# Kernel tuning notes

Measured on AMD Instinct MI355X. Metric: run time of the kernel, lower is better.

Reference implementation:

```python
import jax, jax.numpy as jnp
import numpy as np

D_MODEL = 1024
H = 16
D_K = D_MODEL // H
WINDOW = 256
NEG = -1.0e9


def setup_inputs() -> dict:
    key = jax.random.key(0)
    ks = jax.random.split(key, 12)
    B, S = 1, 4096
    scale = 1.0 / np.sqrt(D_MODEL)
    inp = {
        'q': jax.random.normal(ks[0], (B, S, D_MODEL), dtype=jnp.float32),
        'k': jax.random.normal(ks[1], (B, S, D_MODEL), dtype=jnp.float32),
        'v': jax.random.normal(ks[2], (B, S, D_MODEL), dtype=jnp.float32),
        'w_q': jax.random.normal(ks[3], (D_MODEL, D_MODEL), dtype=jnp.float32) * scale,
        'b_q': jnp.zeros((D_MODEL,), dtype=jnp.float32),
        'w_k': jax.random.normal(ks[4], (D_MODEL, D_MODEL), dtype=jnp.float32) * scale,
        'b_k': jnp.zeros((D_MODEL,), dtype=jnp.float32),
        'w_v': jax.random.normal(ks[5], (D_MODEL, D_MODEL), dtype=jnp.float32) * scale,
        'b_v': jnp.zeros((D_MODEL,), dtype=jnp.float32),
        'w_o': jax.random.normal(ks[6], (D_MODEL, D_MODEL), dtype=jnp.float32) * scale,
        'b_o': jnp.zeros((D_MODEL,), dtype=jnp.float32),
    }
    return inp


def _local_mask(seq_len: int, window_size: int) -> jnp.ndarray:
    left = (window_size - 1) // 2
    right = window_size - 1 - left
    row = jnp.arange(seq_len)[:, None]
    col = jnp.arange(seq_len)[None, :]
    return (col >= row - left) & (col <= row + right)  # [S, S] bool


def reference(q, k, v, w_q, b_q, w_k, b_k, w_v, b_v, w_o, b_o):
    B, Sq, _ = q.shape
    Sk = k.shape[1]
    # projections (torch Linear: x @ W.T + b) -> [B, h, S, d_k]
    query = (q @ w_q.T + b_q).reshape(B, Sq, H, D_K).transpose(0, 2, 1, 3)
    key = (k @ w_k.T + b_k).reshape(B, Sk, H, D_K).transpose(0, 2, 1, 3)
    value = (v @ w_v.T + b_v).reshape(B, Sk, H, D_K).transpose(0, 2, 1, 3)

    scores = jnp.einsum('bhqd,bhkd->bhqk', query, key) / jnp.sqrt(
        jnp.asarray(D_K, dtype=query.dtype))
    if Sq == Sk:
        mask = _local_mask(Sq, WINDOW)  # [S, S]
        scores = jnp.where(mask[None, None], scores, jnp.asarray(NEG, scores.dtype))
    attn = jax.nn.softmax(scores, axis=-1)
    x = jnp.einsum('bhqk,bhkd->bhqd', attn, value)
    x = x.transpose(0, 2, 1, 3).reshape(B, Sq, D_MODEL)
    return x @ w_o.T + b_o
```

## Files before the change

kernel.cpp:

```cpp
#include <hip/hip_runtime.h>

#define SEQ 4096
#define DM 1024
#define NH 16
#define DK 64

typedef _Float16 half8 __attribute__((ext_vector_type(8)));
typedef _Float16 half4v __attribute__((ext_vector_type(4)));
typedef float f32x4 __attribute__((ext_vector_type(4)));

#define MFMA16(a, b, c) __builtin_amdgcn_mfma_f32_16x16x32_f16((a), (b), (c), 0, 0, 0)
#define GLOAD_LDS(g, l)                                                                  \
    __builtin_amdgcn_global_load_lds((const __attribute__((address_space(1))) void*)(g), \
                                     (__attribute__((address_space(3))) void*)(l), 16, 0, 0)

__device__ __forceinline__ float dpp_max16(float x) {
    x = fmaxf(x, __int_as_float(__builtin_amdgcn_update_dpp(
                     0, __float_as_int(x), 0xB1, 0xF, 0xF, true)));
    x = fmaxf(x, __int_as_float(__builtin_amdgcn_update_dpp(
                     0, __float_as_int(x), 0x4E, 0xF, 0xF, true)));
    x = fmaxf(x, __int_as_float(__builtin_amdgcn_update_dpp(
                     0, __float_as_int(x), 0x124, 0xF, 0xF, true)));
    x = fmaxf(x, __int_as_float(__builtin_amdgcn_update_dpp(
                     0, __float_as_int(x), 0x128, 0xF, 0xF, true)));
    return x;
}

__global__ void cvt_all(const float* __restrict__ q, const float* __restrict__ k,
                        const float* __restrict__ v, const float* __restrict__ wq,
                        const float* __restrict__ wk, const float* __restrict__ wv,
                        const float* __restrict__ wo, _Float16* __restrict__ qh,
                        _Float16* __restrict__ kh, _Float16* __restrict__ vh,
                        _Float16* __restrict__ wqh, _Float16* __restrict__ wkh,
                        _Float16* __restrict__ wvh, _Float16* __restrict__ woh) {
    int z = blockIdx.y;
    const float* src;
    _Float16* dst;
    int n;
    switch (z) {
    case 0: src = q;  dst = qh;  n = SEQ * DM; break;
    case 1: src = k;  dst = kh;  n = SEQ * DM; break;
    case 2: src = v;  dst = vh;  n = SEQ * DM; break;
    case 3: src = wq; dst = wqh; n = DM * DM;  break;
    case 4: src = wk; dst = wkh; n = DM * DM;  break;
    case 5: src = wv; dst = wvh; n = DM * DM;  break;
    default: src = wo; dst = woh; n = DM * DM; break;
    }
    int idx = (blockIdx.x * 256 + threadIdx.x) * 8;
    if (idx >= n) return;
    float4 f0 = *(const float4*)(src + idx);
    float4 f1 = *(const float4*)(src + idx + 4);
    half8 h;
    h[0] = (_Float16)f0.x; h[1] = (_Float16)f0.y; h[2] = (_Float16)f0.z; h[3] = (_Float16)f0.w;
    h[4] = (_Float16)f1.x; h[5] = (_Float16)f1.y; h[6] = (_Float16)f1.z; h[7] = (_Float16)f1.w;
    *(half8*)(dst + idx) = h;
}

template <int MT>
__device__ __forceinline__ void gemm_bk64(const _Float16* __restrict__ A,
                                          const _Float16* __restrict__ B, int m0, int n0,
                                          _Float16* As, _Float16* Bs, f32x4 (*acc)[4]) {
    constexpr int MI = MT / 32;
    constexpr int ACH = MT / 64;
    const int tid = threadIdx.x;
    const int wave = tid >> 6, lane = tid & 63;
    const int quad = lane >> 4, l16 = lane & 15;
    const int wr = (wave >> 1) * (MT / 2);
    const int wc = (wave & 1) * 64;
    const int srow = tid >> 2, scol = (tid & 3) * 8;

    for (int k0 = 0; k0 < DM; k0 += 64) {
#pragma unroll
        for (int p = 0; p < 2; ++p) {
            int kc = k0 + p * 32 + scol;
#pragma unroll
            for (int j = 0; j < ACH; ++j)
                GLOAD_LDS(A + (size_t)(m0 + j * 64 + srow) * DM + kc,
                          As + p * (MT * 32) + j * 2048 + tid * 8);
#pragma unroll
            for (int j = 0; j < 2; ++j)
                GLOAD_LDS(B + (size_t)(n0 + j * 64 + srow) * DM + kc,
                          Bs + p * 4096 + j * 2048 + tid * 8);
        }
        __syncthreads();
#pragma unroll
        for (int p = 0; p < 2; ++p) {
            half8 af[MI], bf[4];
#pragma unroll
            for (int mi = 0; mi < MI; ++mi)
                af[mi] = *(const half8*)&As[p * (MT * 32) + (wr + mi * 16 + l16) * 32 + quad * 8];
#pragma unroll
            for (int ni = 0; ni < 4; ++ni)
                bf[ni] = *(const half8*)&Bs[p * 4096 + (wc + ni * 16 + l16) * 32 + quad * 8];
#pragma unroll
            for (int mi = 0; mi < MI; ++mi)
#pragma unroll
                for (int ni = 0; ni < 4; ++ni)
                    acc[mi][ni] = MFMA16(af[mi], bf[ni], acc[mi][ni]);
        }
        __syncthreads();
    }
}

__global__ void __launch_bounds__(256, 3) gemm_qkv(
    const _Float16* __restrict__ qh, const _Float16* __restrict__ kh,
    const _Float16* __restrict__ vh, const _Float16* __restrict__ wqh,
    const _Float16* __restrict__ wkh, const _Float16* __restrict__ wvh,
    const float* __restrict__ bq, const float* __restrict__ bk, const float* __restrict__ bv,
    _Float16* __restrict__ Qo, _Float16* __restrict__ Ko, _Float16* __restrict__ Vt) {
    __shared__ _Float16 As[2 * 128 * 32];
    __shared__ _Float16 Bs[2 * 128 * 32];
    int z = blockIdx.z;
    const _Float16 *A, *B;
    const float* bias;
    float scale;
    if (z == 0) { A = qh; B = wqh; bias = bq; scale = 0.125f; }
    else if (z == 1) { A = kh; B = wkh; bias = bk; scale = 1.0f; }
    else { A = vh; B = wvh; bias = bv; scale = 1.0f; }

    int m0 = blockIdx.x * 128;
    int n0 = blockIdx.y * 128;
    f32x4 acc[4][4] = {};
    gemm_bk64<128>(A, B, m0, n0, As, Bs, acc);

    const int tid = threadIdx.x;
    const int wave = tid >> 6, lane = tid & 63;
    const int quad = lane >> 4, l16 = lane & 15;
    const int wr = (wave >> 1) * 64;
    const int wc = (wave & 1) * 64;
    float bs[4];
#pragma unroll
    for (int ni = 0; ni < 4; ++ni) bs[ni] = bias[n0 + wc + ni * 16 + l16];

    if (z < 2) {
        _Float16* C = (z == 0) ? Qo : Ko;
#pragma unroll
        for (int mi = 0; mi < 4; ++mi)
#pragma unroll
            for (int ni = 0; ni < 4; ++ni) {
                int m = m0 + wr + mi * 16 + quad * 4;
                int n = n0 + wc + ni * 16 + l16;
#pragma unroll
                for (int r = 0; r < 4; ++r)
                    C[(size_t)(m + r) * DM + n] = (_Float16)((acc[mi][ni][r] + bs[ni]) * scale);
            }
    } else {
#pragma unroll
        for (int mi = 0; mi < 4; ++mi)
#pragma unroll
            for (int ni = 0; ni < 4; ++ni) {
                int m = m0 + wr + mi * 16 + quad * 4;
                int n = n0 + wc + ni * 16 + l16;
                half4v p;
#pragma unroll
                for (int r = 0; r < 4; ++r) p[r] = (_Float16)(acc[mi][ni][r] + bs[ni]);
                *(half4v*)(Vt + (size_t)n * SEQ + m) = p;
            }
    }
}

__global__ void __launch_bounds__(256, 3) gemm_out(const _Float16* __restrict__ Xh,
                                                   const _Float16* __restrict__ woh,
                                                   const float* __restrict__ bo,
                                                   float* __restrict__ out) {
    __shared__ _Float16 As[2 * 64 * 32];
    __shared__ _Float16 Bs[2 * 128 * 32];
    int m0 = blockIdx.x * 64;
    int n0 = blockIdx.y * 128;
    f32x4 acc[2][4] = {};
    gemm_bk64<64>(Xh, woh, m0, n0, As, Bs, acc);

    const int tid = threadIdx.x;
    const int wave = tid >> 6, lane = tid & 63;
    const int quad = lane >> 4, l16 = lane & 15;
    const int wr = (wave >> 1) * 32;
    const int wc = (wave & 1) * 64;
#pragma unroll
    for (int mi = 0; mi < 2; ++mi)
#pragma unroll
        for (int ni = 0; ni < 4; ++ni) {
            int m = m0 + wr + mi * 16 + quad * 4;
            int n = n0 + wc + ni * 16 + l16;
            float b = bo[n];
#pragma unroll
            for (int r = 0; r < 4; ++r) out[(size_t)(m + r) * DM + n] = acc[mi][ni][r] + b;
        }
}

__global__ void __launch_bounds__(256, 4) attn_kernel(const _Float16* __restrict__ Q,
                                                      const _Float16* __restrict__ K,
                                                      const _Float16* __restrict__ Vt,
                                                      _Float16* __restrict__ X) {
    __shared__ _Float16 Ks[320 * 64];
    __shared__ _Float16 Pl[4][16][40];
    __shared__ _Float16 Vs[2][64][32];
    int tid = threadIdx.x;
    int wave = tid >> 6, lane = tid & 63;
    int quad = lane >> 4, l16 = lane & 15;
    int h = blockIdx.y;
    int bx = ((blockIdx.x & 7) << 3) + (blockIdx.x >> 3);
    int q0b = bx * 64;
    int q0 = q0b + wave * 16;
    int kspan0 = q0b - 128;

    const _Float16* Kg = K + h * DK;
#pragma unroll
    for (int i = 0; i < 10; ++i) {
        int U = i * 256 + tid;
        int row = U >> 3, u = U & 7;
        int rg = kspan0 + row;
        rg = rg < 0 ? 0 : (rg > SEQ - 1 ? SEQ - 1 : rg);
        GLOAD_LDS(Kg + (size_t)rg * DM + ((u ^ (row & 7)) << 3), Ks + U * 8);
    }

    int ustart = (q0b > 127) ? (q0b - 128) : 0;
    int uend = q0b + 191;
    if (uend > SEQ - 1) uend = SEQ - 1;
    int nt = ((uend - ustart) >> 5) + 1;

    const _Float16* Vg = Vt + (size_t)(h * DK) * SEQ;
    const int vdd = tid >> 2, vu = (tid & 3) * 8;
    GLOAD_LDS(Vg + (size_t)vdd * SEQ + ustart + vu, (_Float16*)Vs + tid * 8);

    const _Float16* Qp = Q + (size_t)(q0 + l16) * DM + h * DK + quad * 8;
    half8 aq0 = *(const half8*)(Qp);
    half8 aq1 = *(const half8*)(Qp + 32);
    const half8 ones = {(_Float16)1, (_Float16)1, (_Float16)1, (_Float16)1,
                        (_Float16)1, (_Float16)1, (_Float16)1, (_Float16)1};

    float rowM[4], rowL[4];
    f32x4 o[4] = {};
#pragma unroll
    for (int r = 0; r < 4; ++r) { rowM[r] = -__builtin_inff(); rowL[r] = 0.f; }

    const int xk = l16 & 7;

    __syncthreads();

    for (int i = 0; i < nt; ++i) {
        int kt = ustart + i * 32;
        int buf = i & 1;
        if (i > 0) {
            asm volatile("s_waitcnt vmcnt(0)" ::: "memory");
            asm volatile("s_barrier" ::: "memory");
        }
        if (i + 1 < nt)
            GLOAD_LDS(Vg + (size_t)vdd * SEQ + (kt + 32) + vu,
                      (_Float16*)Vs + (buf ^ 1) * 2048 + tid * 8);

        int rel = kt - kspan0;
        f32x4 s[2];
#pragma unroll
        for (int cf = 0; cf < 2; ++cf) {
            int rr = rel + cf * 16 + l16;
            half8 b0 = *(const half8*)&Ks[rr * 64 + ((quad ^ xk) << 3)];
            half8 b1 = *(const half8*)&Ks[rr * 64 + (((quad + 4) ^ xk) << 3)];
            f32x4 z = {};
            z = MFMA16(aq0, b0, z);
            z = MFMA16(aq1, b1, z);
            s[cf] = z;
        }
        const bool full = (kt >= q0 - 112) && (kt <= q0 + 97);
        float alpha[4];
#pragma unroll
        for (int r = 0; r < 4; ++r) {
            float x0 = s[0][r], x1 = s[1][r];
            if (!full) {
                int row = q0 + quad * 4 + r;
                int key0 = kt + l16, key1 = kt + 16 + l16;
                if (key0 < row - 127 || key0 > row + 128) x0 = -1e30f;
                if (key1 < row - 127 || key1 > row + 128) x1 = -1e30f;
            }
            float t = dpp_max16(fmaxf(x0, x1));
            float mnew = fmaxf(rowM[r], t);
            alpha[r] = __expf(rowM[r] - mnew);
            float p0 = __expf(x0 - mnew);
            float p1 = __expf(x1 - mnew);
            Pl[wave][quad * 4 + r][l16] = (_Float16)p0;
            Pl[wave][quad * 4 + r][l16 + 16] = (_Float16)p1;
            rowM[r] = mnew;
        }
        half8 ap = *(const half8*)&Pl[wave][l16][quad * 8];
        f32x4 ts = {};
        ts = MFMA16(ap, ones, ts);
#pragma unroll
        for (int r = 0; r < 4; ++r) rowL[r] = rowL[r] * alpha[r] + ts[r];
#pragma unroll
        for (int ni = 0; ni < 4; ++ni) {
#pragma unroll
            for (int r = 0; r < 4; ++r) o[ni][r] *= alpha[r];
            half8 bv = *(const half8*)&Vs[buf][ni * 16 + l16][quad * 8];
            o[ni] = MFMA16(ap, bv, o[ni]);
        }
    }

    float rinv[4];
#pragma unroll
    for (int r = 0; r < 4; ++r) rinv[r] = 1.0f / rowL[r];
#pragma unroll
    for (int ni = 0; ni < 4; ++ni) {
        int n = h * DK + ni * 16 + l16;
#pragma unroll
        for (int r = 0; r < 4; ++r) {
            int m = q0 + quad * 4 + r;
            X[(size_t)m * DM + n] = (_Float16)(o[ni][r] * rinv[r]);
        }
    }
}

extern "C" void kernel_launch(void* const* d_in, const int* in_sizes, int n_in, void* d_out,
                              int out_size, void* d_ws, size_t ws_size, hipStream_t stream) {
    const float* q  = (const float*)d_in[0];
    const float* k  = (const float*)d_in[1];
    const float* v  = (const float*)d_in[2];
    const float* wq = (const float*)d_in[3];
    const float* bq = (const float*)d_in[4];
    const float* wk = (const float*)d_in[5];
    const float* bk = (const float*)d_in[6];
    const float* wv = (const float*)d_in[7];
    const float* bv = (const float*)d_in[8];
    const float* wo = (const float*)d_in[9];
    const float* bo = (const float*)d_in[10];

    const size_t SZ_T = (size_t)SEQ * DM * sizeof(_Float16);
    const size_t SZ_W = (size_t)DM * DM * sizeof(_Float16);
    char* p = (char*)d_ws;
    _Float16* qh  = (_Float16*)(p);
    _Float16* kh  = (_Float16*)(p + SZ_T);
    _Float16* vh  = (_Float16*)(p + 2 * SZ_T);
    _Float16* wqh = (_Float16*)(p + 3 * SZ_T);
    _Float16* wkh = (_Float16*)(p + 3 * SZ_T + SZ_W);
    _Float16* wvh = (_Float16*)(p + 3 * SZ_T + 2 * SZ_W);
    _Float16* woh = (_Float16*)(p + 3 * SZ_T + 3 * SZ_W);
    _Float16* Qo  = (_Float16*)(p + 3 * SZ_T + 4 * SZ_W);
    _Float16* Ko  = (_Float16*)(p + 4 * SZ_T + 4 * SZ_W);
    _Float16* Vt  = (_Float16*)(p + 5 * SZ_T + 4 * SZ_W);
    _Float16* Xh  = qh;

    cvt_all<<<dim3(2048, 7), 256, 0, stream>>>(q, k, v, wq, wk, wv, wo, qh, kh, vh, wqh, wkh,
                                               wvh, woh);
    gemm_qkv<<<dim3(32, 8, 3), 256, 0, stream>>>(qh, kh, vh, wqh, wkh, wvh, bq, bk, bv, Qo, Ko,
                                                 Vt);
    attn_kernel<<<dim3(SEQ / 64, NH), 256, 0, stream>>>(Qo, Ko, Vt, Xh);
    gemm_out<<<dim3(64, 8), 256, 0, stream>>>(Xh, woh, bo, (float*)d_out);
}
```

Before: 192.9 us.

## Fuse fp32-to-fp16 conversion into GEMM tile loads, drop conversion kernel

Removes the separate cvt_all pass. The QKV and output GEMMs now load fp32 tiles directly into LDS with an XOR swizzle and convert them to fp16 in registers just before the MFMA. This avoids writing and rereading fp16 copies of the inputs and weights, and saves one kernel launch. In exchange, each GEMM moves twice as many bytes per tile through global memory and LDS, the K-step shrinks to 32, and the conversion is redone for every tile reuse across blocks.

```diff
diff --git a/kernel.cpp b/kernel.cpp
--- a/kernel.cpp
+++ b/kernel.cpp
@@ -26,108 +26,75 @@
     return x;
 }
 
-__global__ void cvt_all(const float* __restrict__ q, const float* __restrict__ k,
-                        const float* __restrict__ v, const float* __restrict__ wq,
-                        const float* __restrict__ wk, const float* __restrict__ wv,
-                        const float* __restrict__ wo, _Float16* __restrict__ qh,
-                        _Float16* __restrict__ kh, _Float16* __restrict__ vh,
-                        _Float16* __restrict__ wqh, _Float16* __restrict__ wkh,
-                        _Float16* __restrict__ wvh, _Float16* __restrict__ woh) {
-    int z = blockIdx.y;
-    const float* src;
-    _Float16* dst;
-    int n;
-    switch (z) {
-    case 0: src = q;  dst = qh;  n = SEQ * DM; break;
-    case 1: src = k;  dst = kh;  n = SEQ * DM; break;
-    case 2: src = v;  dst = vh;  n = SEQ * DM; break;
-    case 3: src = wq; dst = wqh; n = DM * DM;  break;
-    case 4: src = wk; dst = wkh; n = DM * DM;  break;
-    case 5: src = wv; dst = wvh; n = DM * DM;  break;
-    default: src = wo; dst = woh; n = DM * DM; break;
-    }
-    int idx = (blockIdx.x * 256 + threadIdx.x) * 8;
-    if (idx >= n) return;
-    float4 f0 = *(const float4*)(src + idx);
-    float4 f1 = *(const float4*)(src + idx + 4);
+__device__ __forceinline__ half8 cvt_f32x8(f32x4 lo, f32x4 hi) {
     half8 h;
-    h[0] = (_Float16)f0.x; h[1] = (_Float16)f0.y; h[2] = (_Float16)f0.z; h[3] = (_Float16)f0.w;
-    h[4] = (_Float16)f1.x; h[5] = (_Float16)f1.y; h[6] = (_Float16)f1.z; h[7] = (_Float16)f1.w;
-    *(half8*)(dst + idx) = h;
-}
-
-template <int MT>
-__device__ __forceinline__ void gemm_bk64(const _Float16* __restrict__ A,
-                                          const _Float16* __restrict__ B, int m0, int n0,
-                                          _Float16* As, _Float16* Bs, f32x4 (*acc)[4]) {
-    constexpr int MI = MT / 32;
-    constexpr int ACH = MT / 64;
-    const int tid = threadIdx.x;
-    const int wave = tid >> 6, lane = tid & 63;
-    const int quad = lane >> 4, l16 = lane & 15;
-    const int wr = (wave >> 1) * (MT / 2);
-    const int wc = (wave & 1) * 64;
-    const int srow = tid >> 2, scol = (tid & 3) * 8;
-
-    for (int k0 = 0; k0 < DM; k0 += 64) {
-#pragma unroll
-        for (int p = 0; p < 2; ++p) {
-            int kc = k0 + p * 32 + scol;
-#pragma unroll
-            for (int j = 0; j < ACH; ++j)
-                GLOAD_LDS(A + (size_t)(m0 + j * 64 + srow) * DM + kc,
-                          As + p * (MT * 32) + j * 2048 + tid * 8);
-#pragma unroll
-            for (int j = 0; j < 2; ++j)
-                GLOAD_LDS(B + (size_t)(n0 + j * 64 + srow) * DM + kc,
-                          Bs + p * 4096 + j * 2048 + tid * 8);
-        }
-        __syncthreads();
-#pragma unroll
-        for (int p = 0; p < 2; ++p) {
-            half8 af[MI], bf[4];
-#pragma unroll
-            for (int mi = 0; mi < MI; ++mi)
-                af[mi] = *(const half8*)&As[p * (MT * 32) + (wr + mi * 16 + l16) * 32 + quad * 8];
-#pragma unroll
-            for (int ni = 0; ni < 4; ++ni)
-                bf[ni] = *(const half8*)&Bs[p * 4096 + (wc + ni * 16 + l16) * 32 + quad * 8];
-#pragma unroll
-            for (int mi = 0; mi < MI; ++mi)
-#pragma unroll
-                for (int ni = 0; ni < 4; ++ni)
-                    acc[mi][ni] = MFMA16(af[mi], bf[ni], acc[mi][ni]);
-        }
-        __syncthreads();
-    }
+    h[0] = (_Float16)lo[0]; h[1] = (_Float16)lo[1];
+    h[2] = (_Float16)lo[2]; h[3] = (_Float16)lo[3];
+    h[4] = (_Float16)hi[0]; h[5] = (_Float16)hi[1];
+    h[6] = (_Float16)hi[2]; h[7] = (_Float16)hi[3];
+    return h;
 }
 
 __global__ void __launch_bounds__(256, 3) gemm_qkv(
-    const _Float16* __restrict__ qh, const _Float16* __restrict__ kh,
-    const _Float16* __restrict__ vh, const _Float16* __restrict__ wqh,
-    const _Float16* __restrict__ wkh, const _Float16* __restrict__ wvh,
+    const float* __restrict__ q, const float* __restrict__ k, const float* __restrict__ v,
+    const float* __restrict__ wq, const float* __restrict__ wk, const float* __restrict__ wv,
     const float* __restrict__ bq, const float* __restrict__ bk, const float* __restrict__ bv,
     _Float16* __restrict__ Qo, _Float16* __restrict__ Ko, _Float16* __restrict__ Vt) {
-    __shared__ _Float16 As[2 * 128 * 32];
-    __shared__ _Float16 Bs[2 * 128 * 32];
+    __shared__ float As[128 * 32];
+    __shared__ float Bs[128 * 32];
     int z = blockIdx.z;
-    const _Float16 *A, *B;
-    const float* bias;
+    const float *A, *B, *bias;
     float scale;
-    if (z == 0) { A = qh; B = wqh; bias = bq; scale = 0.125f; }
-    else if (z == 1) { A = kh; B = wkh; bias = bk; scale = 1.0f; }
-    else { A = vh; B = wvh; bias = bv; scale = 1.0f; }
-
-    int m0 = blockIdx.x * 128;
-    int n0 = blockIdx.y * 128;
-    f32x4 acc[4][4] = {};
-    gemm_bk64<128>(A, B, m0, n0, As, Bs, acc);
-
+    if (z == 0) { A = q; B = wq; bias = bq; scale = 0.125f; }
+    else if (z == 1) { A = k; B = wk; bias = bk; scale = 1.0f; }
+    else { A = v; B = wv; bias = bv; scale = 1.0f; }
+
+    const int m0 = blockIdx.x * 128;
+    const int n0 = blockIdx.y * 128;
     const int tid = threadIdx.x;
     const int wave = tid >> 6, lane = tid & 63;
     const int quad = lane >> 4, l16 = lane & 15;
     const int wr = (wave >> 1) * 64;
     const int wc = (wave & 1) * 64;
+    const int s7 = l16 & 7;
+
+    f32x4 acc[4][4] = {};
+
+    for (int k0 = 0; k0 < DM; k0 += 32) {
+#pragma unroll
+        for (int i = 0; i < 4; ++i) {
+            int U = i * 256 + tid;
+            int row = U >> 3, u = U & 7;
+            int c = k0 + ((u ^ (row & 7)) << 2);
+            GLOAD_LDS(A + (size_t)(m0 + row) * DM + c, As + U * 4);
+            GLOAD_LDS(B + (size_t)(n0 + row) * DM + c, Bs + U * 4);
+        }
+        __syncthreads();
+
+        half8 ah[4], bh[4];
+        const int u0 = (2 * quad) ^ s7;
+#pragma unroll
+        for (int mi = 0; mi < 4; ++mi) {
+            int row = wr + mi * 16 + l16;
+            f32x4 lo = *(const f32x4*)&As[row * 32 + u0 * 4];
+            f32x4 hi = *(const f32x4*)&As[row * 32 + (u0 ^ 1) * 4];
+            ah[mi] = cvt_f32x8(lo, hi);
+        }
+#pragma unroll
+        for (int ni = 0; ni < 4; ++ni) {
+            int row = wc + ni * 16 + l16;
+            f32x4 lo = *(const f32x4*)&Bs[row * 32 + u0 * 4];
+            f32x4 hi = *(const f32x4*)&Bs[row * 32 + (u0 ^ 1) * 4];
+            bh[ni] = cvt_f32x8(lo, hi);
+        }
+#pragma unroll
+        for (int mi = 0; mi < 4; ++mi)
+#pragma unroll
+            for (int ni = 0; ni < 4; ++ni)
+                acc[mi][ni] = MFMA16(ah[mi], bh[ni], acc[mi][ni]);
+        __syncthreads();
+    }
+
     float bs[4];
 #pragma unroll
     for (int ni = 0; ni < 4; ++ni) bs[ni] = bias[n0 + wc + ni * 16 + l16];
@@ -160,21 +127,60 @@
 }
 
 __global__ void __launch_bounds__(256, 3) gemm_out(const _Float16* __restrict__ Xh,
-                                                   const _Float16* __restrict__ woh,
+                                                   const float* __restrict__ wo,
                                                    const float* __restrict__ bo,
                                                    float* __restrict__ out) {
-    __shared__ _Float16 As[2 * 64 * 32];
-    __shared__ _Float16 Bs[2 * 128 * 32];
-    int m0 = blockIdx.x * 64;
-    int n0 = blockIdx.y * 128;
-    f32x4 acc[2][4] = {};
-    gemm_bk64<64>(Xh, woh, m0, n0, As, Bs, acc);
-
+    __shared__ _Float16 As[64 * 32];
+    __shared__ float Bs[128 * 32];
+    const int m0 = blockIdx.x * 64;
+    const int n0 = blockIdx.y * 128;
     const int tid = threadIdx.x;
     const int wave = tid >> 6, lane = tid & 63;
     const int quad = lane >> 4, l16 = lane & 15;
     const int wr = (wave >> 1) * 32;
     const int wc = (wave & 1) * 64;
+    const int s7 = l16 & 7;
+
+    f32x4 acc[2][4] = {};
+
+    for (int k0 = 0; k0 < DM; k0 += 32) {
+        {
+            int row = tid >> 2, u = tid & 3;
+            int c = k0 + ((u ^ (row & 3)) << 3);
+            GLOAD_LDS(Xh + (size_t)(m0 + row) * DM + c, As + tid * 8);
+        }
+#pragma unroll
+        for (int i = 0; i < 4; ++i) {
+            int U = i * 256 + tid;
+            int row = U >> 3, u = U & 7;
+            int c = k0 + ((u ^ (row & 7)) << 2);
+            GLOAD_LDS(wo + (size_t)(n0 + row) * DM + c, Bs + U * 4);
+        }
+        __syncthreads();
+
+        half8 ah[2], bh[4];
+        const int ua = quad ^ (l16 & 3);
+#pragma unroll
+        for (int mi = 0; mi < 2; ++mi) {
+            int row = wr + mi * 16 + l16;
+            ah[mi] = *(const half8*)&As[row * 32 + ua * 8];
+        }
+        const int u0 = (2 * quad) ^ s7;
+#pragma unroll
+        for (int ni = 0; ni < 4; ++ni) {
+            int row = wc + ni * 16 + l16;
+            f32x4 lo = *(const f32x4*)&Bs[row * 32 + u0 * 4];
+            f32x4 hi = *(const f32x4*)&Bs[row * 32 + (u0 ^ 1) * 4];
+            bh[ni] = cvt_f32x8(lo, hi);
+        }
+#pragma unroll
+        for (int mi = 0; mi < 2; ++mi)
+#pragma unroll
+            for (int ni = 0; ni < 4; ++ni)
+                acc[mi][ni] = MFMA16(ah[mi], bh[ni], acc[mi][ni]);
+        __syncthreads();
+    }
+
 #pragma unroll
     for (int mi = 0; mi < 2; ++mi)
 #pragma unroll
@@ -323,24 +329,13 @@
     const float* bo = (const float*)d_in[10];
 
     const size_t SZ_T = (size_t)SEQ * DM * sizeof(_Float16);
-    const size_t SZ_W = (size_t)DM * DM * sizeof(_Float16);
     char* p = (char*)d_ws;
-    _Float16* qh  = (_Float16*)(p);
-    _Float16* kh  = (_Float16*)(p + SZ_T);
-    _Float16* vh  = (_Float16*)(p + 2 * SZ_T);
-    _Float16* wqh = (_Float16*)(p + 3 * SZ_T);
-    _Float16* wkh = (_Float16*)(p + 3 * SZ_T + SZ_W);
-    _Float16* wvh = (_Float16*)(p + 3 * SZ_T + 2 * SZ_W);
-    _Float16* woh = (_Float16*)(p + 3 * SZ_T + 3 * SZ_W);
-    _Float16* Qo  = (_Float16*)(p + 3 * SZ_T + 4 * SZ_W);
-    _Float16* Ko  = (_Float16*)(p + 4 * SZ_T + 4 * SZ_W);
-    _Float16* Vt  = (_Float16*)(p + 5 * SZ_T + 4 * SZ_W);
-    _Float16* Xh  = qh;
-
-    cvt_all<<<dim3(2048, 7), 256, 0, stream>>>(q, k, v, wq, wk, wv, wo, qh, kh, vh, wqh, wkh,
-                                               wvh, woh);
-    gemm_qkv<<<dim3(32, 8, 3), 256, 0, stream>>>(qh, kh, vh, wqh, wkh, wvh, bq, bk, bv, Qo, Ko,
-                                                 Vt);
+    _Float16* Qo = (_Float16*)(p);
+    _Float16* Ko = (_Float16*)(p + SZ_T);
+    _Float16* Vt = (_Float16*)(p + 2 * SZ_T);
+    _Float16* Xh = (_Float16*)(p + 3 * SZ_T);
+
+    gemm_qkv<<<dim3(32, 8, 3), 256, 0, stream>>>(q, k, v, wq, wk, wv, bq, bk, bv, Qo, Ko, Vt);
     attn_kernel<<<dim3(SEQ / 64, NH), 256, 0, stream>>>(Qo, Ko, Vt, Xh);
-    gemm_out<<<dim3(64, 8), 256, 0, stream>>>(Xh, woh, bo, (float*)d_out);
-}
+    gemm_out<<<dim3(64, 8), 256, 0, stream>>>(Xh, wo, bo, (float*)d_out);
+}
```

Result: slower. 215.9 us (+11.9%).
